# Kernel optimization log

Hardware: AMD Instinct MI355X
Metric: run time of the kernel (lower is better)

## Reference

```python
import jax, jax.numpy as jnp
import numpy as np

B, N, D = 2048, 65536, 128  # batch queries, max_engrams, spike_dim


def setup_inputs() -> dict:
    key = jax.random.key(0)
    k1, k2, k3, k4 = jax.random.split(key, 4)
    sensor_spikes = jax.random.normal(k1, (B, D), dtype=jnp.float32)
    # crystallize_skill stores sign(pattern), so keys/values are +-1 vectors
    sensor_keys = jnp.sign(jax.random.normal(k2, (N, D), dtype=jnp.float32))
    action_values = jnp.sign(jax.random.normal(k3, (N, D), dtype=jnp.float32))
    is_active = jax.random.bernoulli(k4, 0.5, (N,))
    return {
        "sensor_spikes": sensor_spikes,
        "sensor_keys": sensor_keys,
        "action_values": action_values,
        "is_active": is_active,
    }


def reference(sensor_spikes, sensor_keys, action_values, is_active):
    # similarity = x @ keys.T  -> [B, N]
    sim = jnp.einsum("bd,nd->bn", sensor_spikes.astype(jnp.float32), sensor_keys)
    # masked_fill_(~is_active, -inf)
    sim = jnp.where(is_active[None, :], sim, -jnp.inf)
    best_match_idx = jnp.argmax(sim, axis=-1)          # [B]
    confidence = jnp.max(sim, axis=-1)                 # [B] == sim[b, best_idx[b]]
    retrieved = action_values[best_match_idx]          # [B, D]
    return retrieved, confidence, best_match_idx
```

## Files before the change

### kernel.cpp

```cpp
#include <hip/hip_runtime.h>
#include <stdint.h>

typedef __attribute__((ext_vector_type(8))) short short8;
typedef __attribute__((ext_vector_type(4))) float f32x4;

#define NEG_INF (-__builtin_inff())

#define B_ROWS 2048
#define N_KEYS 65536
#define DIM    128


__device__ __forceinline__ unsigned short f2bf(float f) {
  unsigned u = __float_as_uint(f);
  u = (u + 0x7FFFu + ((u >> 16) & 1u)) >> 16;
  return (unsigned short)u;
}


__global__ __launch_bounds__(256) void convert_x_kernel(
    const float* __restrict__ x, short8* __restrict__ xi) {
  int t = blockIdx.x * 256 + threadIdx.x;
  int tile = t >> 11, loc = t & 2047;
  int rl = ((loc >> 8) << 4) + (loc & 15);
  int c = (loc >> 4) & 15;
  const float* src = x + (size_t)(tile * 128 + rl) * DIM + c * 8;
  f32x4 v0 = *(const f32x4*)(src);
  f32x4 v1 = *(const f32x4*)(src + 4);
  short8 o;
  o[0] = (short)f2bf(v0[0]); o[1] = (short)f2bf(v0[1]);
  o[2] = (short)f2bf(v0[2]); o[3] = (short)f2bf(v0[3]);
  o[4] = (short)f2bf(v1[0]); o[5] = (short)f2bf(v1[1]);
  o[6] = (short)f2bf(v1[2]); o[7] = (short)f2bf(v1[3]);
  xi[t] = o;
}

#define GLDS(gp, lp)                                                      \
  __builtin_amdgcn_global_load_lds(                                       \
      (const __attribute__((address_space(1))) void*)(gp),                \
      (__attribute__((address_space(3))) void*)(lp), 16, 0, 0)

__global__ __launch_bounds__(256, 2) void sim2_kernel(
    const short8* __restrict__ xi, const float* __restrict__ keys,
    const int* __restrict__ act, float* __restrict__ cmaxT) {
  __shared__ short8 Bs[2048];
  __shared__ short8 As[2048];
  __shared__ float actm[128];
  const int tid = threadIdx.x;
  const int w = tid >> 6, l = tid & 63;
  const int ntile = blockIdx.x;

  const float* kb = keys + (size_t)ntile * (128 * DIM);
#pragma unroll
  for (int it = 0; it < 8; ++it) {
    int li = it * 256 + tid;
    int rl = ((li >> 8) << 4) + (li & 15);
    int c = (li >> 4) & 15;
    const float* src = kb + rl * DIM + c * 8;
    f32x4 v0 = *(const f32x4*)(src);
    f32x4 v1 = *(const f32x4*)(src + 4);
    short8 o;
    o[0] = (short)f2bf(v0[0]); o[1] = (short)f2bf(v0[1]);
    o[2] = (short)f2bf(v0[2]); o[3] = (short)f2bf(v0[3]);
    o[4] = (short)f2bf(v1[0]); o[5] = (short)f2bf(v1[1]);
    o[6] = (short)f2bf(v1[2]); o[7] = (short)f2bf(v1[3]);
    Bs[li] = o;
  }
  if (tid < 128) {
    actm[tid] = act[ntile * 128 + tid] ? 0.0f : NEG_INF;
  }

  const int wr = w >> 1, wc = w & 1;
  const int lg = l >> 4, lr = l & 15;
  const short8* ag0 = xi + w * 512 + l;
  float* cout = cmaxT + (size_t)(ntile * 2 + wc) * B_ROWS;

  for (int bt = 0; bt < 16; ++bt) {
    __syncthreads();
    const short8* ag = ag0 + (size_t)bt * 2048;
#pragma unroll
    for (int i = 0; i < 8; i++)
      GLDS(ag + i * 64, As + w * 512 + i * 64);
    __syncthreads();

    f32x4 acc[4][4];
#pragma unroll
    for (int mi = 0; mi < 4; mi++)
#pragma unroll
      for (int ni = 0; ni < 4; ni++) acc[mi][ni] = f32x4{0.f, 0.f, 0.f, 0.f};

#pragma unroll
    for (int kk = 0; kk < 4; kk++) {
      short8 af[4], bfv[4];
#pragma unroll
      for (int mi = 0; mi < 4; mi++) af[mi] = As[(wr * 4 + mi) * 256 + kk * 64 + l];
#pragma unroll
      for (int ni = 0; ni < 4; ni++) bfv[ni] = Bs[(wc * 4 + ni) * 256 + kk * 64 + l];
#pragma unroll
      for (int mi = 0; mi < 4; mi++)
#pragma unroll
        for (int ni = 0; ni < 4; ni++)
          acc[mi][ni] = __builtin_amdgcn_mfma_f32_16x16x32_bf16(
              af[mi], bfv[ni], acc[mi][ni], 0, 0, 0);
    }

#pragma unroll
    for (int mi = 0; mi < 4; mi++) {
      float rm[4];
#pragma unroll
      for (int r = 0; r < 4; r++) rm[r] = NEG_INF;
#pragma unroll
      for (int ni = 0; ni < 4; ni++) {
        float m = actm[wc * 64 + ni * 16 + lr];
#pragma unroll
        for (int r = 0; r < 4; r++) rm[r] = fmaxf(rm[r], acc[mi][ni][r] + m);
      }
#pragma unroll
      for (int r = 0; r < 4; r++) {
        float v = rm[r];
        v = fmaxf(v, __shfl_xor(v, 1));
        v = fmaxf(v, __shfl_xor(v, 2));
        v = fmaxf(v, __shfl_xor(v, 4));
        v = fmaxf(v, __shfl_xor(v, 8));
        rm[r] = v;
      }
      if (lr == 0) {
        int row = bt * 128 + wr * 64 + mi * 16 + lg * 4;
        *(f32x4*)(cout + row) = f32x4{rm[0], rm[1], rm[2], rm[3]};
      }
    }
  }
}

__global__ __launch_bounds__(256) void finalize_kernel(
    const float* __restrict__ x, const float* __restrict__ keys,
    const float* __restrict__ vals, const int* __restrict__ act,
    const float* __restrict__ cmaxT, float* __restrict__ out) {
  __shared__ float xr[128];
  __shared__ float wred[4];
  __shared__ int cand[64];
  __shared__ int ncand;
  __shared__ int bestn_s;
  __shared__ float skeys[64 * 129];
  const int b = blockIdx.x, tid = threadIdx.x;
  if (tid < 128) xr[tid] = x[(size_t)b * 128 + tid];
  if (tid == 0) ncand = 0;
  __syncthreads();

  const float* cm = cmaxT + b;
  float c0 = cm[(size_t)tid * B_ROWS];
  float c1 = cm[(size_t)(tid + 256) * B_ROWS];
  float c2 = cm[(size_t)(tid + 512) * B_ROWS];
  float c3 = cm[(size_t)(tid + 768) * B_ROWS];
  float lm = fmaxf(fmaxf(c0, c1), fmaxf(c2, c3));
#pragma unroll
  for (int s = 1; s < 64; s <<= 1) lm = fmaxf(lm, __shfl_xor(lm, s));
  if ((tid & 63) == 0) wred[tid >> 6] = lm;
  __syncthreads();
  float M = fmaxf(fmaxf(wred[0], wred[1]), fmaxf(wred[2], wred[3]));
  float thr = M - 0.75f;

  if (c0 > thr) { int p = atomicAdd(&ncand, 1); if (p < 64) cand[p] = tid; }
  if (c1 > thr) { int p = atomicAdd(&ncand, 1); if (p < 64) cand[p] = tid + 256; }
  if (c2 > thr) { int p = atomicAdd(&ncand, 1); if (p < 64) cand[p] = tid + 512; }
  if (c3 > thr) { int p = atomicAdd(&ncand, 1); if (p < 64) cand[p] = tid + 768; }
  __syncthreads();
  int nc = ncand; if (nc > 64) nc = 64;

  double bv = -(double)__builtin_inf();
  int bn = 0x7FFFFFFF;
  for (int ci = 0; ci < nc; ci++) {
    int cch = cand[ci];
    const float* kbase = keys + (size_t)cch * 64 * 128;
#pragma unroll
    for (int i = 0; i < 32; i++) {
      int idx = tid + i * 256;
      skeys[(idx >> 7) * 129 + (idx & 127)] = kbase[idx];
    }
    __syncthreads();
    if (tid < 64) {
      int n = cch * 64 + tid;
      if (act[n] != 0) {
        const float* kr = skeys + tid * 129;
        double s = 0.0;
#pragma unroll
        for (int d = 0; d < 128; d++) s += (double)xr[d] * (double)kr[d];
        if (s > bv || (s == bv && n < bn)) { bv = s; bn = n; }
      }
    }
    __syncthreads();
  }

  if (tid < 64) {
#pragma unroll
    for (int s = 1; s < 64; s <<= 1) {
      double ov = __shfl_xor(bv, s);
      int on = __shfl_xor(bn, s);
      if (ov > bv || (ov == bv && on < bn)) { bv = ov; bn = on; }
    }
    if (tid == 0) {
      bestn_s = bn;
      out[262144 + b] = (float)bv;
      out[264192 + b] = (float)bn;
    }
  }
  __syncthreads();
  int n = bestn_s;
  if (tid < 128) out[(size_t)b * 128 + tid] = vals[(size_t)n * 128 + tid];
}

__global__ __launch_bounds__(256) void direct_kernel(
    const float* __restrict__ x, const float* __restrict__ keys,
    const float* __restrict__ vals, const int* __restrict__ act,
    float* __restrict__ out) {
  __shared__ float xr[8][128];
  __shared__ double redv[8][4];
  __shared__ int redn[8][4];
  __shared__ int bests[8];
  const int tid = threadIdx.x;
  const int r0 = blockIdx.x * 8;
  const int w = tid >> 6, l = tid & 63;
#pragma unroll
  for (int i = 0; i < 4; i++) {
    int idx = tid + i * 256;
    xr[idx >> 7][idx & 127] = x[(size_t)(r0 + (idx >> 7)) * 128 + (idx & 127)];
  }
  __syncthreads();

  double bv[8];
  int bn[8];
#pragma unroll
  for (int r = 0; r < 8; r++) { bv[r] = -(double)__builtin_inf(); bn[r] = 0x7FFFFFFF; }

  for (int n = tid; n < N_KEYS; n += 256) {
    if (act[n] == 0) continue;
    const float* kr = keys + (size_t)n * 128;
    double s[8];
#pragma unroll
    for (int r = 0; r < 8; r++) s[r] = 0.0;
    for (int d = 0; d < 128; d += 4) {
      f32x4 kv = *(const f32x4*)(kr + d);
#pragma unroll
      for (int r = 0; r < 8; r++) {
        s[r] += (double)xr[r][d] * (double)kv[0];
        s[r] += (double)xr[r][d + 1] * (double)kv[1];
        s[r] += (double)xr[r][d + 2] * (double)kv[2];
        s[r] += (double)xr[r][d + 3] * (double)kv[3];
      }
    }
#pragma unroll
    for (int r = 0; r < 8; r++)
      if (s[r] > bv[r]) { bv[r] = s[r]; bn[r] = n; }
  }

#pragma unroll
  for (int r = 0; r < 8; r++) {
    double v = bv[r]; int n = bn[r];
#pragma unroll
    for (int s = 1; s < 64; s <<= 1) {
      double ov = __shfl_xor(v, s);
      int on = __shfl_xor(n, s);
      if (ov > v || (ov == v && on < n)) { v = ov; n = on; }
    }
    if (l == 0) { redv[r][w] = v; redn[r][w] = n; }
  }
  __syncthreads();
  if (tid < 8) {
    double v = redv[tid][0]; int n = redn[tid][0];
#pragma unroll
    for (int j = 1; j < 4; j++) {
      double ov = redv[tid][j]; int on = redn[tid][j];
      if (ov > v || (ov == v && on < n)) { v = ov; n = on; }
    }
    bests[tid] = n;
    out[262144 + r0 + tid] = (float)v;
    out[264192 + r0 + tid] = (float)n;
  }
  __syncthreads();
#pragma unroll
  for (int i = 0; i < 4; i++) {
    int idx = tid + i * 256;
    int r = idx >> 7, d = idx & 127;
    out[(size_t)(r0 + r) * 128 + d] = vals[(size_t)bests[r] * 128 + d];
  }
}

extern "C" void kernel_launch(void* const* d_in, const int* in_sizes, int n_in,
                              void* d_out, int out_size, void* d_ws, size_t ws_size,
                              hipStream_t stream) {
  const float* x    = (const float*)d_in[0];
  const float* keys = (const float*)d_in[1];
  const float* vals = (const float*)d_in[2];
  const int*   act  = (const int*)d_in[3];
  float* out = (float*)d_out;

  const size_t need = (size_t)16 * 2048 * sizeof(short8) +
                      (size_t)1024 * B_ROWS * sizeof(float);
  if (ws_size >= need) {
    short8* xi    = (short8*)d_ws;
    float*  cmaxT = (float*)(xi + 16 * 2048);
    convert_x_kernel<<<128, 256, 0, stream>>>(x, xi);
    sim2_kernel<<<512, 256, 0, stream>>>(xi, keys, act, cmaxT);
    finalize_kernel<<<2048, 256, 0, stream>>>(x, keys, vals, act, cmaxT, out);
  } else {
    direct_kernel<<<256, 256, 0, stream>>>(x, keys, vals, act, out);
  }
}
```

Before: 181.6 us.

## Keep key fragments in registers, read query fragments from global, fold mask into keys

The similarity kernel now keeps its B fragments (bf16 keys) in registers for the whole block. A fragments are read straight from global memory each batch tile, replacing the LDS staging and the two barriers per tile. Inactive keys are zeroed in the bf16 copy instead of getting a -inf mask added, so inactive chunks score 0 rather than -inf; the exact fp64 rescoring in finalize still skips inactive keys, and the candidate list grows to 96. Per-chunk maxima are stored row-major so finalize reads them contiguously, and the fp64 dot product uses four accumulators to shorten its dependency chain.

```diff
diff --git a/kernel.cpp b/kernel.cpp
--- a/kernel.cpp
+++ b/kernel.cpp
@@ -35,17 +35,10 @@
   xi[t] = o;
 }
 
-#define GLDS(gp, lp)                                                      \
-  __builtin_amdgcn_global_load_lds(                                       \
-      (const __attribute__((address_space(1))) void*)(gp),                \
-      (__attribute__((address_space(3))) void*)(lp), 16, 0, 0)
-
-__global__ __launch_bounds__(256, 2) void sim2_kernel(
+__global__ __launch_bounds__(256, 2) void sim3_kernel(
     const short8* __restrict__ xi, const float* __restrict__ keys,
-    const int* __restrict__ act, float* __restrict__ cmaxT) {
+    const int* __restrict__ act, float* __restrict__ cmax) {
   __shared__ short8 Bs[2048];
-  __shared__ short8 As[2048];
-  __shared__ float actm[128];
   const int tid = threadIdx.x;
   const int w = tid >> 6, l = tid & 63;
   const int ntile = blockIdx.x;
@@ -59,29 +52,37 @@
     const float* src = kb + rl * DIM + c * 8;
     f32x4 v0 = *(const f32x4*)(src);
     f32x4 v1 = *(const f32x4*)(src + 4);
+    int a = act[ntile * 128 + rl];
     short8 o;
     o[0] = (short)f2bf(v0[0]); o[1] = (short)f2bf(v0[1]);
     o[2] = (short)f2bf(v0[2]); o[3] = (short)f2bf(v0[3]);
     o[4] = (short)f2bf(v1[0]); o[5] = (short)f2bf(v1[1]);
     o[6] = (short)f2bf(v1[2]); o[7] = (short)f2bf(v1[3]);
+    if (!a) o = short8{0, 0, 0, 0, 0, 0, 0, 0};
     Bs[li] = o;
   }
-  if (tid < 128) {
-    actm[tid] = act[ntile * 128 + tid] ? 0.0f : NEG_INF;
-  }
+  __syncthreads();
 
   const int wr = w >> 1, wc = w & 1;
   const int lg = l >> 4, lr = l & 15;
-  const short8* ag0 = xi + w * 512 + l;
-  float* cout = cmaxT + (size_t)(ntile * 2 + wc) * B_ROWS;
+
+  short8 bfv[4][4];
+#pragma unroll
+  for (int ni = 0; ni < 4; ni++)
+#pragma unroll
+    for (int kk = 0; kk < 4; kk++)
+      bfv[ni][kk] = Bs[(wc * 4 + ni) * 256 + kk * 64 + l];
+
+  const int chunk = ntile * 2 + wc;
+  const short8* ag0 = xi + (wr * 4) * 256 + l;
 
   for (int bt = 0; bt < 16; ++bt) {
-    __syncthreads();
-    const short8* ag = ag0 + (size_t)bt * 2048;
-#pragma unroll
-    for (int i = 0; i < 8; i++)
-      GLDS(ag + i * 64, As + w * 512 + i * 64);
-    __syncthreads();
+    short8 af[4][4];
+#pragma unroll
+    for (int mi = 0; mi < 4; mi++)
+#pragma unroll
+      for (int kk = 0; kk < 4; kk++)
+        af[mi][kk] = ag0[(size_t)bt * 2048 + mi * 256 + kk * 64];
 
     f32x4 acc[4][4];
 #pragma unroll
@@ -90,31 +91,21 @@
       for (int ni = 0; ni < 4; ni++) acc[mi][ni] = f32x4{0.f, 0.f, 0.f, 0.f};
 
 #pragma unroll
-    for (int kk = 0; kk < 4; kk++) {
-      short8 af[4], bfv[4];
-#pragma unroll
-      for (int mi = 0; mi < 4; mi++) af[mi] = As[(wr * 4 + mi) * 256 + kk * 64 + l];
-#pragma unroll
-      for (int ni = 0; ni < 4; ni++) bfv[ni] = Bs[(wc * 4 + ni) * 256 + kk * 64 + l];
+    for (int kk = 0; kk < 4; kk++)
 #pragma unroll
       for (int mi = 0; mi < 4; mi++)
 #pragma unroll
         for (int ni = 0; ni < 4; ni++)
           acc[mi][ni] = __builtin_amdgcn_mfma_f32_16x16x32_bf16(
-              af[mi], bfv[ni], acc[mi][ni], 0, 0, 0);
-    }
+              af[mi][kk], bfv[ni][kk], acc[mi][ni], 0, 0, 0);
 
 #pragma unroll
     for (int mi = 0; mi < 4; mi++) {
       float rm[4];
 #pragma unroll
-      for (int r = 0; r < 4; r++) rm[r] = NEG_INF;
-#pragma unroll
-      for (int ni = 0; ni < 4; ni++) {
-        float m = actm[wc * 64 + ni * 16 + lr];
-#pragma unroll
-        for (int r = 0; r < 4; r++) rm[r] = fmaxf(rm[r], acc[mi][ni][r] + m);
-      }
+      for (int r = 0; r < 4; r++)
+        rm[r] = fmaxf(fmaxf(acc[mi][0][r], acc[mi][1][r]),
+                      fmaxf(acc[mi][2][r], acc[mi][3][r]));
 #pragma unroll
       for (int r = 0; r < 4; r++) {
         float v = rm[r];
@@ -126,7 +117,9 @@
       }
       if (lr == 0) {
         int row = bt * 128 + wr * 64 + mi * 16 + lg * 4;
-        *(f32x4*)(cout + row) = f32x4{rm[0], rm[1], rm[2], rm[3]};
+#pragma unroll
+        for (int r = 0; r < 4; r++)
+          cmax[(size_t)(row + r) * 1024 + chunk] = rm[r];
       }
     }
   }
@@ -135,10 +128,10 @@
 __global__ __launch_bounds__(256) void finalize_kernel(
     const float* __restrict__ x, const float* __restrict__ keys,
     const float* __restrict__ vals, const int* __restrict__ act,
-    const float* __restrict__ cmaxT, float* __restrict__ out) {
+    const float* __restrict__ cmax, float* __restrict__ out) {
   __shared__ float xr[128];
   __shared__ float wred[4];
-  __shared__ int cand[64];
+  __shared__ int cand[96];
   __shared__ int ncand;
   __shared__ int bestn_s;
   __shared__ float skeys[64 * 129];
@@ -147,11 +140,8 @@
   if (tid == 0) ncand = 0;
   __syncthreads();
 
-  const float* cm = cmaxT + b;
-  float c0 = cm[(size_t)tid * B_ROWS];
-  float c1 = cm[(size_t)(tid + 256) * B_ROWS];
-  float c2 = cm[(size_t)(tid + 512) * B_ROWS];
-  float c3 = cm[(size_t)(tid + 768) * B_ROWS];
+  const float* cm = cmax + (size_t)b * 1024;
+  float c0 = cm[tid], c1 = cm[tid + 256], c2 = cm[tid + 512], c3 = cm[tid + 768];
   float lm = fmaxf(fmaxf(c0, c1), fmaxf(c2, c3));
 #pragma unroll
   for (int s = 1; s < 64; s <<= 1) lm = fmaxf(lm, __shfl_xor(lm, s));
@@ -160,12 +150,12 @@
   float M = fmaxf(fmaxf(wred[0], wred[1]), fmaxf(wred[2], wred[3]));
   float thr = M - 0.75f;
 
-  if (c0 > thr) { int p = atomicAdd(&ncand, 1); if (p < 64) cand[p] = tid; }
-  if (c1 > thr) { int p = atomicAdd(&ncand, 1); if (p < 64) cand[p] = tid + 256; }
-  if (c2 > thr) { int p = atomicAdd(&ncand, 1); if (p < 64) cand[p] = tid + 512; }
-  if (c3 > thr) { int p = atomicAdd(&ncand, 1); if (p < 64) cand[p] = tid + 768; }
-  __syncthreads();
-  int nc = ncand; if (nc > 64) nc = 64;
+  if (c0 > thr) { int p = atomicAdd(&ncand, 1); if (p < 96) cand[p] = tid; }
+  if (c1 > thr) { int p = atomicAdd(&ncand, 1); if (p < 96) cand[p] = tid + 256; }
+  if (c2 > thr) { int p = atomicAdd(&ncand, 1); if (p < 96) cand[p] = tid + 512; }
+  if (c3 > thr) { int p = atomicAdd(&ncand, 1); if (p < 96) cand[p] = tid + 768; }
+  __syncthreads();
+  int nc = ncand; if (nc > 96) nc = 96;
 
   double bv = -(double)__builtin_inf();
   int bn = 0x7FFFFFFF;
@@ -182,9 +172,15 @@
       int n = cch * 64 + tid;
       if (act[n] != 0) {
         const float* kr = skeys + tid * 129;
-        double s = 0.0;
-#pragma unroll
-        for (int d = 0; d < 128; d++) s += (double)xr[d] * (double)kr[d];
+        double s0 = 0.0, s1 = 0.0, s2 = 0.0, s3 = 0.0;
+#pragma unroll
+        for (int d = 0; d < 128; d += 4) {
+          s0 += (double)xr[d] * (double)kr[d];
+          s1 += (double)xr[d + 1] * (double)kr[d + 1];
+          s2 += (double)xr[d + 2] * (double)kr[d + 2];
+          s3 += (double)xr[d + 3] * (double)kr[d + 3];
+        }
+        double s = (s0 + s1) + (s2 + s3);
         if (s > bv || (s == bv && n < bn)) { bv = s; bn = n; }
       }
     }
@@ -295,13 +291,13 @@
   float* out = (float*)d_out;
 
   const size_t need = (size_t)16 * 2048 * sizeof(short8) +
-                      (size_t)1024 * B_ROWS * sizeof(float);
+                      (size_t)B_ROWS * 1024 * sizeof(float);
   if (ws_size >= need) {
-    short8* xi    = (short8*)d_ws;
-    float*  cmaxT = (float*)(xi + 16 * 2048);
+    short8* xi   = (short8*)d_ws;
+    float*  cmax = (float*)(xi + 16 * 2048);
     convert_x_kernel<<<128, 256, 0, stream>>>(x, xi);
-    sim2_kernel<<<512, 256, 0, stream>>>(xi, keys, act, cmaxT);
-    finalize_kernel<<<2048, 256, 0, stream>>>(x, keys, vals, act, cmaxT, out);
+    sim3_kernel<<<512, 256, 0, stream>>>(xi, keys, act, cmax);
+    finalize_kernel<<<2048, 256, 0, stream>>>(x, keys, vals, act, cmax, out);
   } else {
     direct_kernel<<<256, 256, 0, stream>>>(x, keys, vals, act, out);
   }
```

New measurement: 178.2 us. Within noise of the previous version (-1.9%).
